# Optimization experiments

Hardware: AMD Instinct MI355X
Metric: run time of the kernel (lower is better)

## Reference

```python
import jax, jax.numpy as jnp
import numpy as np

NU = 20000; NI = 20000; E = 200000; H = 8; D = 64; F = H * D
B = 1024; P = 8; K = 8


def gat(h, W, al, ar, b, src, dst, N):
    # DGL GATConv (eval mode, dropout off): fc -> edge attention -> edge softmax -> scatter-sum -> bias -> elu
    f = (h @ W).reshape(N, H, D)                       # [N,H,D]
    el = jnp.einsum('nhd,hd->nh', f, al)               # [N,H]
    er = jnp.einsum('nhd,hd->nh', f, ar)
    e = jax.nn.leaky_relu(el[src] + er[dst], 0.2)      # [E,H]
    m = jax.ops.segment_max(e, dst, num_segments=N)    # [N,H]
    m = jnp.where(jnp.isfinite(m), m, 0.0)             # nodes w/ zero in-degree
    ex = jnp.exp(e - m[dst])                           # [E,H]
    s = jax.ops.segment_sum(ex, dst, num_segments=N)   # [N,H]
    alpha = ex / jnp.maximum(s[dst], 1e-9)             # [E,H]
    out = jax.ops.segment_sum(alpha[:, :, None] * f[src], dst, num_segments=N)  # [N,H,D]
    return jax.nn.elu(out.reshape(N, F) + b)


def semantic_attention(z, W1, b1, v):
    # z: [N, M, F]
    w = jnp.mean(jnp.tanh(z @ W1 + b1) @ v, axis=0)    # [M]
    beta = jax.nn.softmax(w)
    return jnp.einsum('m,nmf->nf', beta, z)


def han_layer(h, Wg, al, ar, bg, W1, b1, v, src, dst, N):
    zs = [gat(h, Wg[i], al[i], ar[i], bg[i], src[i], dst[i], N) for i in range(Wg.shape[0])]
    return semantic_attention(jnp.stack(zs, axis=1), W1, b1, v)


def setup_inputs() -> dict:
    key = jax.random.key(0)
    ks = jax.random.split(key, 24)
    sc = 0.05
    return {
        'user_embs': jax.random.normal(ks[0], (NU, D), jnp.float32) * sc,
        'item_embs': jax.random.normal(ks[1], (NI, D), jnp.float32) * sc,
        'Wg_u': jax.random.normal(ks[2], (2, D, F), jnp.float32) * sc,
        'al_u': jax.random.normal(ks[3], (2, H, D), jnp.float32) * sc,
        'ar_u': jax.random.normal(ks[4], (2, H, D), jnp.float32) * sc,
        'bg_u': jax.random.normal(ks[5], (2, F), jnp.float32) * sc,
        'Ws_u': jax.random.normal(ks[6], (F, 128), jnp.float32) * sc,
        'bs_u': jax.random.normal(ks[7], (128,), jnp.float32) * sc,
        'vs_u': jax.random.normal(ks[8], (128,), jnp.float32) * sc,
        'Wg_i': jax.random.normal(ks[9], (2, D, F), jnp.float32) * sc,
        'al_i': jax.random.normal(ks[10], (2, H, D), jnp.float32) * sc,
        'ar_i': jax.random.normal(ks[11], (2, H, D), jnp.float32) * sc,
        'bg_i': jax.random.normal(ks[12], (2, F), jnp.float32) * sc,
        'Ws_i': jax.random.normal(ks[13], (F, 128), jnp.float32) * sc,
        'bs_i': jax.random.normal(ks[14], (128,), jnp.float32) * sc,
        'vs_i': jax.random.normal(ks[15], (128,), jnp.float32) * sc,
        'src_u': jax.random.randint(ks[16], (2, E), 0, NU, jnp.int32),
        'dst_u': jax.random.randint(ks[17], (2, E), 0, NU, jnp.int32),
        'src_i': jax.random.randint(ks[18], (2, E), 0, NI, jnp.int32),
        'dst_i': jax.random.randint(ks[19], (2, E), 0, NI, jnp.int32),
        'uid': jax.random.randint(ks[20], (B,), 0, NU, jnp.int32),
        'pos': jax.random.randint(ks[21], (B, P), 0, NI, jnp.int32),
        'neg': jax.random.randint(ks[22], (B, P, K), 0, NI, jnp.int32),
    }


def reference(user_embs, item_embs, Wg_u, al_u, ar_u, bg_u, Ws_u, bs_u, vs_u,
              Wg_i, al_i, ar_i, bg_i, Ws_i, bs_i, vs_i,
              src_u, dst_u, src_i, dst_i, uid, pos, neg):
    hu = han_layer(user_embs, Wg_u, al_u, ar_u, bg_u, Ws_u, bs_u, vs_u, src_u, dst_u, NU)  # [NU,F]
    hi = han_layer(item_embs, Wg_i, al_i, ar_i, bg_i, Ws_i, bs_i, vs_i, src_i, dst_i, NI)  # [NI,F]
    ue = hu[uid]                                     # [B,F]
    pe = hi[pos]                                     # [B,P,F]
    ne = hi[neg]                                     # [B,P,K,F]
    ue_p = jnp.broadcast_to(ue[:, None, :], pe.shape)
    pos_logits = (ue_p * pe).sum(-1)[..., None]      # [B,P,1]
    ue_n = jnp.broadcast_to(ue_p[:, :, None, :], ne.shape)
    neg_logits = (ue_n * ne).sum(-1)                 # [B,P,K]
    return pos_logits, neg_logits, ue_n, pe, ne
```

## Files before the change

### kernel.cpp

```cpp
#include <hip/hip_runtime.h>
#include <hip/hip_bf16.h>
#include <cstddef>

#define NN 20000
#define EE 200000

typedef __attribute__((ext_vector_type(8))) short bf8_t;
typedef __attribute__((ext_vector_type(4))) float f32x4;

__device__ __forceinline__ float bf2f(unsigned int lo16) {
    return __uint_as_float(lo16 << 16);
}
__device__ __forceinline__ unsigned short f2bf(float f) {
    unsigned u = __float_as_uint(f);
    u += 0x7fffu + ((u >> 16) & 1u);
    return (unsigned short)(u >> 16);
}

__global__ void prep_kernel(
    const float* __restrict__ user_embs, const float* __restrict__ item_embs,
    const float* __restrict__ Wg_u, const float* __restrict__ Wg_i,
    const float* __restrict__ Ws_u, const float* __restrict__ Ws_i,
    unsigned short* __restrict__ hb,
    unsigned short* __restrict__ Wt,
    unsigned short* __restrict__ W1t)
{
    int i = blockIdx.x * 256 + threadIdx.x;
    if (i < 2 * NN * 64) {
        float v = (i < NN * 64) ? user_embs[i] : item_embs[i - NN * 64];
        hb[i] = f2bf(v);
    }
    if (i < 4 * 512 * 64) {
        int tg = i >> 15, rem = i & 32767;
        int col = rem >> 6, k = rem & 63;
        const float* W = (tg < 2 ? Wg_u + tg * 32768 : Wg_i + (tg - 2) * 32768);
        Wt[i] = f2bf(W[k * 512 + col]);
    }
    if (i < 2 * 128 * 512) {
        int t = i >> 16, rem = i & 65535;
        int c = rem >> 9, k = rem & 511;
        const float* Wsrc = t ? Ws_i : Ws_u;
        W1t[i] = f2bf(Wsrc[k * 128 + c]);
    }
}

__global__ __launch_bounds__(256) void fc_kernel(
    const unsigned short* __restrict__ hb,
    const unsigned short* __restrict__ Wt,
    const float* __restrict__ al_u, const float* __restrict__ ar_u,
    const float* __restrict__ al_i, const float* __restrict__ ar_i,
    unsigned short* __restrict__ fb,
    float* __restrict__ el, float* __restrict__ er)
{
    const int tg = blockIdx.y, t = tg >> 1, g = tg & 1;
    const int tid = threadIdx.x, wid = tid >> 6, lane = tid & 63;
    const int r0 = blockIdx.x * 16;
    const unsigned short* A = hb + (size_t)t * NN * 64;
    const unsigned short* B = Wt + (size_t)tg * 512 * 64;
    const float* alf = (t ? al_i : al_u) + g * 512;
    const float* arf = (t ? ar_i : ar_u) + g * 512;

    const int arow = lane & 15, ak0 = (lane >> 4) * 8;
    const bf8_t a0 = *(const bf8_t*)(A + (size_t)(r0 + arow) * 64 + ak0);
    const bf8_t a1 = *(const bf8_t*)(A + (size_t)(r0 + arow) * 64 + 32 + ak0);

    f32x4 acc[8];
#pragma unroll
    for (int i = 0; i < 8; ++i) acc[i] = f32x4{0.f, 0.f, 0.f, 0.f};

#pragma unroll
    for (int tn = 0; tn < 8; ++tn) {
        const unsigned short* bp =
            B + (size_t)(wid * 128 + tn * 16 + (lane & 15)) * 64 + ak0;
        bf8_t b0 = *(const bf8_t*)(bp);
        bf8_t b1 = *(const bf8_t*)(bp + 32);
        acc[tn] = __builtin_amdgcn_mfma_f32_16x16x32_bf16(a0, b0, acc[tn], 0, 0, 0);
        acc[tn] = __builtin_amdgcn_mfma_f32_16x16x32_bf16(a1, b1, acc[tn], 0, 0, 0);
    }

    float elp[2][4], erp[2][4];
#pragma unroll
    for (int hs = 0; hs < 2; ++hs)
#pragma unroll
        for (int r = 0; r < 4; ++r) { elp[hs][r] = 0.f; erp[hs][r] = 0.f; }

#pragma unroll
    for (int tn = 0; tn < 8; ++tn) {
        const int hs = tn >> 2;
        const int col = wid * 128 + tn * 16 + (lane & 15);
        const float av = alf[col], rv = arf[col];
#pragma unroll
        for (int r = 0; r < 4; ++r) {
            elp[hs][r] += acc[tn][r] * av;
            erp[hs][r] += acc[tn][r] * rv;
        }
    }
#pragma unroll
    for (int m = 1; m < 16; m <<= 1) {
#pragma unroll
        for (int hs = 0; hs < 2; ++hs)
#pragma unroll
            for (int r = 0; r < 4; ++r) {
                elp[hs][r] += __shfl_xor(elp[hs][r], m, 64);
                erp[hs][r] += __shfl_xor(erp[hs][r], m, 64);
            }
    }
    if ((lane & 15) == 0) {
        float* elg = el + (size_t)tg * NN * 8;
        float* erg = er + (size_t)tg * NN * 8;
#pragma unroll
        for (int r = 0; r < 4; ++r) {
            const int n = r0 + (lane >> 4) * 4 + r;
            elg[n * 8 + 2 * wid + 0] = elp[0][r];
            elg[n * 8 + 2 * wid + 1] = elp[1][r];
            erg[n * 8 + 2 * wid + 0] = erp[0][r];
            erg[n * 8 + 2 * wid + 1] = erp[1][r];
        }
    }

    __shared__ unsigned short sf[16][512];
#pragma unroll
    for (int tn = 0; tn < 8; ++tn)
#pragma unroll
        for (int r = 0; r < 4; ++r)
            sf[(lane >> 4) * 4 + r][wid * 128 + tn * 16 + (lane & 15)] =
                f2bf(acc[tn][r]);
    __syncthreads();
    unsigned short* fo = fb + (size_t)tg * NN * 512;
#pragma unroll
    for (int s = 0; s < 4; ++s) {
        int ch = tid + s * 256;
        int row = ch >> 6, off = (ch & 63) * 8;
        *(uint4*)(fo + (size_t)(r0 + row) * 512 + off) = *(uint4*)&sf[row][off];
    }
}

__global__ void zero_kernel(int* __restrict__ count, int* __restrict__ cursor,
                            float* __restrict__ wsum)
{
    int i = blockIdx.x * 256 + threadIdx.x;
    if (i < 4 * NN) { count[i] = 0; cursor[i] = 0; }
    if (i < 4) wsum[i] = 0.f;
}

__global__ void hist_kernel(const int* __restrict__ dst_u,
                            const int* __restrict__ dst_i,
                            int* __restrict__ count)
{
    int g = blockIdx.y;
    int i = blockIdx.x * 256 + threadIdx.x;
    if (i < EE) {
        const int* d = (g < 2 ? dst_u : dst_i) + (size_t)(g & 1) * EE;
        atomicAdd(&count[g * NN + d[i]], 1);
    }
}

__global__ __launch_bounds__(256) void scan1_kernel(
    const int* __restrict__ count, int* __restrict__ tmp,
    int* __restrict__ partials)
{
    const int g = blockIdx.y, tid = threadIdx.x;
    const int i = blockIdx.x * 256 + tid;
    __shared__ int sc[256];
    int v = (i < NN) ? count[g * NN + i] : 0;
    sc[tid] = v;
    __syncthreads();
#pragma unroll
    for (int off = 1; off < 256; off <<= 1) {
        int add = (tid >= off) ? sc[tid - off] : 0;
        __syncthreads();
        sc[tid] += add;
        __syncthreads();
    }
    if (i < NN) tmp[g * NN + i] = sc[tid] - v;
    if (tid == 255) partials[g * 79 + blockIdx.x] = sc[255];
}

__global__ __launch_bounds__(256) void scan2_kernel(
    const int* __restrict__ partials, int* __restrict__ bases)
{
    __shared__ int p[320], bl[320];
    const int tid = threadIdx.x;
    for (int i = tid; i < 316; i += 256) p[i] = partials[i];
    __syncthreads();
    if (tid < 4) {
        int base = 0;
        for (int b = 0; b < 79; ++b) { bl[tid * 79 + b] = base; base += p[tid * 79 + b]; }
    }
    __syncthreads();
    for (int i = tid; i < 316; i += 256) bases[i] = bl[i];
}

__global__ void scan3_kernel(const int* __restrict__ tmp,
                             const int* __restrict__ bases,
                             int* __restrict__ roff)
{
    const int g = blockIdx.y;
    const int i = blockIdx.x * 256 + threadIdx.x;
    if (i < NN) roff[g * (NN + 1) + i] = tmp[g * NN + i] + bases[g * 79 + blockIdx.x];
    if (blockIdx.x == 0 && threadIdx.x == 0) roff[g * (NN + 1) + NN] = EE;
}

__global__ void scatter_kernel(const int* __restrict__ src_u,
                               const int* __restrict__ dst_u,
                               const int* __restrict__ src_i,
                               const int* __restrict__ dst_i,
                               const int* __restrict__ roff,
                               int* __restrict__ cursor,
                               int* __restrict__ csrc)
{
    int g = blockIdx.y;
    int i = blockIdx.x * 256 + threadIdx.x;
    if (i < EE) {
        const int* s = (g < 2 ? src_u : src_i) + (size_t)(g & 1) * EE;
        const int* d = (g < 2 ? dst_u : dst_i) + (size_t)(g & 1) * EE;
        int dd = d[i];
        int pp = atomicAdd(&cursor[g * NN + dd], 1);
        csrc[(size_t)g * EE + roff[g * (NN + 1) + dd] + pp] = s[i];
    }
}

__global__ __launch_bounds__(256) void agg_kernel(
    const unsigned short* __restrict__ fb,
    const float* __restrict__ el, const float* __restrict__ er,
    const int* __restrict__ roff, const int* __restrict__ csrc,
    const float* __restrict__ bg_u, const float* __restrict__ bg_i,
    unsigned short* __restrict__ zb)
{
    const int tg = blockIdx.y, t = tg >> 1, g = tg & 1;
    const int tid = threadIdx.x, wid = tid >> 6, lane = tid & 63;
    const int n = blockIdx.x * 4 + wid;
    const unsigned short* fg = fb + (size_t)tg * NN * 512;
    const float* elg = el + (size_t)tg * NN * 8;
    const float* erg = er + (size_t)tg * NN * 8;
    const int* ro = roff + (size_t)tg * (NN + 1);
    const int* cs = csrc + (size_t)tg * EE;
    const float* bias = (t ? bg_i : bg_u) + g * 512;

    const int h = lane >> 3, c0 = lane * 8;
    const float ern = erg[n * 8 + h];
    const int beg = ro[n], end = ro[n + 1];

    float s = 0.f;
    float a0 = 0.f, a1 = 0.f, a2 = 0.f, a3 = 0.f, a4 = 0.f, a5 = 0.f, a6 = 0.f, a7 = 0.f;
    for (int e = beg; e < end; ++e) {
        int src = cs[e];
        float x = elg[src * 8 + h] + ern;
        x = (x >= 0.f) ? x : 0.2f * x;
        float ex = __expf(x);
        s += ex;
        uint4 fv = *(const uint4*)(fg + (size_t)src * 512 + c0);
        a0 += ex * bf2f(fv.x & 0xffffu);  a1 += ex * __uint_as_float(fv.x & 0xffff0000u);
        a2 += ex * bf2f(fv.y & 0xffffu);  a3 += ex * __uint_as_float(fv.y & 0xffff0000u);
        a4 += ex * bf2f(fv.z & 0xffffu);  a5 += ex * __uint_as_float(fv.z & 0xffff0000u);
        a6 += ex * bf2f(fv.w & 0xffffu);  a7 += ex * __uint_as_float(fv.w & 0xffff0000u);
    }
    const float inv = 1.f / fmaxf(s, 1e-9f);
    const float4 bA = *(const float4*)(bias + c0);
    const float4 bB = *(const float4*)(bias + c0 + 4);
    float o0 = a0 * inv + bA.x; o0 = o0 > 0.f ? o0 : expm1f(o0);
    float o1 = a1 * inv + bA.y; o1 = o1 > 0.f ? o1 : expm1f(o1);
    float o2 = a2 * inv + bA.z; o2 = o2 > 0.f ? o2 : expm1f(o2);
    float o3 = a3 * inv + bA.w; o3 = o3 > 0.f ? o3 : expm1f(o3);
    float o4 = a4 * inv + bB.x; o4 = o4 > 0.f ? o4 : expm1f(o4);
    float o5 = a5 * inv + bB.y; o5 = o5 > 0.f ? o5 : expm1f(o5);
    float o6 = a6 * inv + bB.z; o6 = o6 > 0.f ? o6 : expm1f(o6);
    float o7 = a7 * inv + bB.w; o7 = o7 > 0.f ? o7 : expm1f(o7);
    uint4 pk;
    pk.x = ((unsigned)f2bf(o1) << 16) | f2bf(o0);
    pk.y = ((unsigned)f2bf(o3) << 16) | f2bf(o2);
    pk.z = ((unsigned)f2bf(o5) << 16) | f2bf(o4);
    pk.w = ((unsigned)f2bf(o7) << 16) | f2bf(o6);
    *(uint4*)(zb + (size_t)tg * NN * 512 + (size_t)n * 512 + c0) = pk;
}

__global__ __launch_bounds__(256) void sem_kernel(
    const unsigned short* __restrict__ zb,
    const unsigned short* __restrict__ W1t,
    const float* __restrict__ bs_u, const float* __restrict__ vs_u,
    const float* __restrict__ bs_i, const float* __restrict__ vs_i,
    float* __restrict__ wsum)
{
    const int tm = blockIdx.y, t = tm >> 1;
    const int tid = threadIdx.x, wid = tid >> 6, lane = tid & 63;
    const int r0 = blockIdx.x * 32;
    const unsigned short* Az = zb + (size_t)tm * NN * 512;
    const unsigned short* Bw = W1t + (size_t)t * 128 * 512;
    const float* b1f = t ? bs_i : bs_u;
    const float* vf  = t ? vs_i : vs_u;

    const int arow = lane & 15, ak0 = (lane >> 4) * 8;
    const int col0 = wid * 32 + (lane & 15);
    const unsigned short* a0p = Az + (size_t)(r0 + arow) * 512 + ak0;
    const unsigned short* a1p = a0p + 16 * 512;
    const unsigned short* b0p = Bw + (size_t)col0 * 512 + ak0;
    const unsigned short* b1p = b0p + 16 * 512;

    f32x4 acc00 = f32x4{0.f,0.f,0.f,0.f}, acc01 = acc00, acc10 = acc00, acc11 = acc00;
#pragma unroll 4
    for (int k = 0; k < 512; k += 32) {
        bf8_t a0 = *(const bf8_t*)(a0p + k);
        bf8_t a1 = *(const bf8_t*)(a1p + k);
        bf8_t b0 = *(const bf8_t*)(b0p + k);
        bf8_t b1 = *(const bf8_t*)(b1p + k);
        acc00 = __builtin_amdgcn_mfma_f32_16x16x32_bf16(a0, b0, acc00, 0, 0, 0);
        acc01 = __builtin_amdgcn_mfma_f32_16x16x32_bf16(a0, b1, acc01, 0, 0, 0);
        acc10 = __builtin_amdgcn_mfma_f32_16x16x32_bf16(a1, b0, acc10, 0, 0, 0);
        acc11 = __builtin_amdgcn_mfma_f32_16x16x32_bf16(a1, b1, acc11, 0, 0, 0);
    }

    const float b1c0 = b1f[col0], b1c1 = b1f[col0 + 16];
    const float vc0 = vf[col0],  vc1 = vf[col0 + 16];
    float q = 0.f;
#pragma unroll
    for (int r = 0; r < 4; ++r) {
        q += tanhf(acc00[r] + b1c0) * vc0;
        q += tanhf(acc01[r] + b1c1) * vc1;
        q += tanhf(acc10[r] + b1c0) * vc0;
        q += tanhf(acc11[r] + b1c1) * vc1;
    }
#pragma unroll
    for (int m = 1; m < 64; m <<= 1) q += __shfl_xor(q, m, 64);
    __shared__ float red[4];
    if (lane == 0) red[wid] = q;
    __syncthreads();
    if (tid == 0) atomicAdd(&wsum[tm], red[0] + red[1] + red[2] + red[3]);
}

__global__ void combine_kernel(const unsigned short* __restrict__ zb,
                               const float* __restrict__ wsum,
                               float* __restrict__ hu, float* __restrict__ hi)
{
    const int t = blockIdx.y;
    const float w0 = wsum[2 * t] * (1.f / (float)NN);
    const float w1 = wsum[2 * t + 1] * (1.f / (float)NN);
    const float m = fmaxf(w0, w1);
    const float e0 = __expf(w0 - m), e1 = __expf(w1 - m);
    const float is = 1.f / (e0 + e1);
    const float be0 = e0 * is, be1 = e1 * is;

    const size_t idx = (size_t)blockIdx.x * 256 + threadIdx.x;
    const unsigned short* z0 = zb + (size_t)(2 * t) * NN * 512 + idx * 8;
    const unsigned short* z1 = zb + (size_t)(2 * t + 1) * NN * 512 + idx * 8;
    float* ho = (t ? hi : hu) + idx * 8;
    uint4 u0 = *(const uint4*)z0;
    uint4 u1 = *(const uint4*)z1;
    float4 oA, oB;
    oA.x = be0 * bf2f(u0.x & 0xffffu) + be1 * bf2f(u1.x & 0xffffu);
    oA.y = be0 * __uint_as_float(u0.x & 0xffff0000u) + be1 * __uint_as_float(u1.x & 0xffff0000u);
    oA.z = be0 * bf2f(u0.y & 0xffffu) + be1 * bf2f(u1.y & 0xffffu);
    oA.w = be0 * __uint_as_float(u0.y & 0xffff0000u) + be1 * __uint_as_float(u1.y & 0xffff0000u);
    oB.x = be0 * bf2f(u0.z & 0xffffu) + be1 * bf2f(u1.z & 0xffffu);
    oB.y = be0 * __uint_as_float(u0.z & 0xffff0000u) + be1 * __uint_as_float(u1.z & 0xffff0000u);
    oB.z = be0 * bf2f(u0.w & 0xffffu) + be1 * bf2f(u1.w & 0xffffu);
    oB.w = be0 * __uint_as_float(u0.w & 0xffff0000u) + be1 * __uint_as_float(u1.w & 0xffff0000u);
    *(float4*)(ho) = oA;
    *(float4*)(ho + 4) = oB;
}

__global__ __launch_bounds__(128) void score_kernel(
    const float* __restrict__ hu, const float* __restrict__ hi,
    const int* __restrict__ uid, const int* __restrict__ pos,
    const int* __restrict__ neg, float* __restrict__ out)
{
    const int bp  = blockIdx.x;
    const int b   = bp >> 3;
    const int tid = threadIdx.x;
    __shared__ float red[2];

    float* pos_logits = out;
    float* neg_logits = out + 8192;
    float* ue_n       = out + 73728;
    float* pe         = out + 33628160;
    float* ne         = out + 37822464;

    const float4 u4 = ((const float4*)(hu + (size_t)uid[b] * 512))[tid];

    {
        const float4 p4 = ((const float4*)(hi + (size_t)pos[bp] * 512))[tid];
        ((float4*)(pe + (size_t)bp * 512))[tid] = p4;
        float d = u4.x * p4.x + u4.y * p4.y + u4.z * p4.z + u4.w * p4.w;
#pragma unroll
        for (int off = 32; off; off >>= 1) d += __shfl_down(d, off, 64);
        if ((tid & 63) == 0) red[tid >> 6] = d;
        __syncthreads();
        if (tid == 0) pos_logits[bp] = red[0] + red[1];
    }
    for (int k = 0; k < 8; ++k) {
        __syncthreads();
        const size_t row = (size_t)bp * 8 + k;
        const float4 n4 = ((const float4*)(hi + (size_t)neg[row] * 512))[tid];
        ((float4*)(ne   + row * 512))[tid] = n4;
        ((float4*)(ue_n + row * 512))[tid] = u4;
        float d = u4.x * n4.x + u4.y * n4.y + u4.z * n4.z + u4.w * n4.w;
#pragma unroll
        for (int off = 32; off; off >>= 1) d += __shfl_down(d, off, 64);
        if ((tid & 63) == 0) red[tid >> 6] = d;
        __syncthreads();
        if (tid == 0) neg_logits[row] = red[0] + red[1];
    }
}

extern "C" void kernel_launch(void* const* d_in, const int* in_sizes, int n_in,
                              void* d_out, int out_size, void* d_ws, size_t ws_size,
                              hipStream_t stream)
{
    const float* user_embs = (const float*)d_in[0];
    const float* item_embs = (const float*)d_in[1];
    const float* Wg_u = (const float*)d_in[2];
    const float* al_u = (const float*)d_in[3];
    const float* ar_u = (const float*)d_in[4];
    const float* bg_u = (const float*)d_in[5];
    const float* Ws_u = (const float*)d_in[6];
    const float* bs_u = (const float*)d_in[7];
    const float* vs_u = (const float*)d_in[8];
    const float* Wg_i = (const float*)d_in[9];
    const float* al_i = (const float*)d_in[10];
    const float* ar_i = (const float*)d_in[11];
    const float* bg_i = (const float*)d_in[12];
    const float* Ws_i = (const float*)d_in[13];
    const float* bs_i = (const float*)d_in[14];
    const float* vs_i = (const float*)d_in[15];
    const int* src_u = (const int*)d_in[16];
    const int* dst_u = (const int*)d_in[17];
    const int* src_i = (const int*)d_in[18];
    const int* dst_i = (const int*)d_in[19];
    const int* uid = (const int*)d_in[20];
    const int* pos = (const int*)d_in[21];
    const int* neg = (const int*)d_in[22];

    char* p = (char*)d_ws;
    auto carve = [&](size_t bytes) {
        char* r = p; p += (bytes + 255) & ~(size_t)255; return r;
    };
    unsigned short* fb  = (unsigned short*)carve((size_t)4 * NN * 512 * 2);
    unsigned short* zb  = (unsigned short*)carve((size_t)4 * NN * 512 * 2);
    unsigned short* hb  = (unsigned short*)carve((size_t)2 * NN * 64 * 2);
    unsigned short* Wt  = (unsigned short*)carve((size_t)4 * 512 * 64 * 2);
    unsigned short* W1t = (unsigned short*)carve((size_t)2 * 128 * 512 * 2);
    float* el   = (float*)carve((size_t)4 * NN * 8 * 4);
    float* er   = (float*)carve((size_t)4 * NN * 8 * 4);
    float* wsum = (float*)carve(64);
    int* count    = (int*)carve((size_t)4 * NN * 4);
    int* cursor   = (int*)carve((size_t)4 * NN * 4);
    int* tmp      = (int*)carve((size_t)4 * NN * 4);
    int* roff     = (int*)carve((size_t)4 * (NN + 1) * 4);
    int* partials = (int*)carve(320 * 4);
    int* bases    = (int*)carve(320 * 4);
    int* csrc     = (int*)carve((size_t)4 * EE * 4);
    float* hu = (float*)fb;
    float* hi = hu + (size_t)NN * 512;

    prep_kernel<<<(2 * NN * 64 + 255) / 256, 256, 0, stream>>>(
        user_embs, item_embs, Wg_u, Wg_i, Ws_u, Ws_i, hb, Wt, W1t);
    zero_kernel<<<(4 * NN + 255) / 256, 256, 0, stream>>>(count, cursor, wsum);
    hist_kernel<<<dim3((EE + 255) / 256, 4), 256, 0, stream>>>(dst_u, dst_i, count);
    scan1_kernel<<<dim3(79, 4), 256, 0, stream>>>(count, tmp, partials);
    scan2_kernel<<<1, 256, 0, stream>>>(partials, bases);
    scan3_kernel<<<dim3(79, 4), 256, 0, stream>>>(tmp, bases, roff);
    scatter_kernel<<<dim3((EE + 255) / 256, 4), 256, 0, stream>>>(
        src_u, dst_u, src_i, dst_i, roff, cursor, csrc);
    fc_kernel<<<dim3(NN / 16, 4), 256, 0, stream>>>(
        hb, Wt, al_u, ar_u, al_i, ar_i, fb, el, er);
    agg_kernel<<<dim3(NN / 4, 4), 256, 0, stream>>>(
        fb, el, er, roff, csrc, bg_u, bg_i, zb);
    sem_kernel<<<dim3(NN / 32, 4), 256, 0, stream>>>(
        zb, W1t, bs_u, vs_u, bs_i, vs_i, wsum);
    combine_kernel<<<dim3(NN * 512 / 8 / 256, 2), 256, 0, stream>>>(zb, wsum, hu, hi);
    score_kernel<<<1024 * 8, 128, 0, stream>>>(hu, hi, uid, pos, neg, (float*)d_out);
}
```

Before: 717.2 us.

## Fuse semantic combine into score kernel and fold zeroing into prep

Removes the combine kernel that built full fp32 hu/hi tables for every node. The score kernel now reads only the gathered rows of the two bf16 metapath embeddings and blends them with the semantic softmax weights on the fly, using one wave per block and no shared-memory reduction. The zero kernel is also merged into prep to save a launch. This avoids writing and re-reading about 80 MB of fp32 node embeddings, at the cost of reading two bf16 rows per gather and recomputing the softmax weights in every block.

```diff
diff --git a/kernel.cpp b/kernel.cpp
--- a/kernel.cpp
+++ b/kernel.cpp
@@ -10,6 +10,9 @@
 
 __device__ __forceinline__ float bf2f(unsigned int lo16) {
     return __uint_as_float(lo16 << 16);
+}
+__device__ __forceinline__ float hi16f(unsigned int u) {
+    return __uint_as_float(u & 0xffff0000u);
 }
 __device__ __forceinline__ unsigned short f2bf(float f) {
     unsigned u = __float_as_uint(f);
@@ -23,7 +26,9 @@
     const float* __restrict__ Ws_u, const float* __restrict__ Ws_i,
     unsigned short* __restrict__ hb,
     unsigned short* __restrict__ Wt,
-    unsigned short* __restrict__ W1t)
+    unsigned short* __restrict__ W1t,
+    int* __restrict__ count, int* __restrict__ cursor,
+    float* __restrict__ wsum)
 {
     int i = blockIdx.x * 256 + threadIdx.x;
     if (i < 2 * NN * 64) {
@@ -42,6 +47,8 @@
         const float* Wsrc = t ? Ws_i : Ws_u;
         W1t[i] = f2bf(Wsrc[k * 128 + c]);
     }
+    if (i < 4 * NN) { count[i] = 0; cursor[i] = 0; }
+    if (i < 4) wsum[i] = 0.f;
 }
 
 __global__ __launch_bounds__(256) void fc_kernel(
@@ -133,14 +140,6 @@
         int row = ch >> 6, off = (ch & 63) * 8;
         *(uint4*)(fo + (size_t)(r0 + row) * 512 + off) = *(uint4*)&sf[row][off];
     }
-}
-
-__global__ void zero_kernel(int* __restrict__ count, int* __restrict__ cursor,
-                            float* __restrict__ wsum)
-{
-    int i = blockIdx.x * 256 + threadIdx.x;
-    if (i < 4 * NN) { count[i] = 0; cursor[i] = 0; }
-    if (i < 4) wsum[i] = 0.f;
 }
 
 __global__ void hist_kernel(const int* __restrict__ dst_u,
@@ -250,10 +249,10 @@
         float ex = __expf(x);
         s += ex;
         uint4 fv = *(const uint4*)(fg + (size_t)src * 512 + c0);
-        a0 += ex * bf2f(fv.x & 0xffffu);  a1 += ex * __uint_as_float(fv.x & 0xffff0000u);
-        a2 += ex * bf2f(fv.y & 0xffffu);  a3 += ex * __uint_as_float(fv.y & 0xffff0000u);
-        a4 += ex * bf2f(fv.z & 0xffffu);  a5 += ex * __uint_as_float(fv.z & 0xffff0000u);
-        a6 += ex * bf2f(fv.w & 0xffffu);  a7 += ex * __uint_as_float(fv.w & 0xffff0000u);
+        a0 += ex * bf2f(fv.x & 0xffffu);  a1 += ex * hi16f(fv.x);
+        a2 += ex * bf2f(fv.y & 0xffffu);  a3 += ex * hi16f(fv.y);
+        a4 += ex * bf2f(fv.z & 0xffffu);  a5 += ex * hi16f(fv.z);
+        a6 += ex * bf2f(fv.w & 0xffffu);  a7 += ex * hi16f(fv.w);
     }
     const float inv = 1.f / fmaxf(s, 1e-9f);
     const float4 bA = *(const float4*)(bias + c0);
@@ -327,46 +326,44 @@
     if (tid == 0) atomicAdd(&wsum[tm], red[0] + red[1] + red[2] + red[3]);
 }
 
-__global__ void combine_kernel(const unsigned short* __restrict__ zb,
-                               const float* __restrict__ wsum,
-                               float* __restrict__ hu, float* __restrict__ hi)
-{
-    const int t = blockIdx.y;
-    const float w0 = wsum[2 * t] * (1.f / (float)NN);
-    const float w1 = wsum[2 * t + 1] * (1.f / (float)NN);
-    const float m = fmaxf(w0, w1);
-    const float e0 = __expf(w0 - m), e1 = __expf(w1 - m);
-    const float is = 1.f / (e0 + e1);
-    const float be0 = e0 * is, be1 = e1 * is;
-
-    const size_t idx = (size_t)blockIdx.x * 256 + threadIdx.x;
-    const unsigned short* z0 = zb + (size_t)(2 * t) * NN * 512 + idx * 8;
-    const unsigned short* z1 = zb + (size_t)(2 * t + 1) * NN * 512 + idx * 8;
-    float* ho = (t ? hi : hu) + idx * 8;
-    uint4 u0 = *(const uint4*)z0;
-    uint4 u1 = *(const uint4*)z1;
-    float4 oA, oB;
-    oA.x = be0 * bf2f(u0.x & 0xffffu) + be1 * bf2f(u1.x & 0xffffu);
-    oA.y = be0 * __uint_as_float(u0.x & 0xffff0000u) + be1 * __uint_as_float(u1.x & 0xffff0000u);
-    oA.z = be0 * bf2f(u0.y & 0xffffu) + be1 * bf2f(u1.y & 0xffffu);
-    oA.w = be0 * __uint_as_float(u0.y & 0xffff0000u) + be1 * __uint_as_float(u1.y & 0xffff0000u);
-    oB.x = be0 * bf2f(u0.z & 0xffffu) + be1 * bf2f(u1.z & 0xffffu);
-    oB.y = be0 * __uint_as_float(u0.z & 0xffff0000u) + be1 * __uint_as_float(u1.z & 0xffff0000u);
-    oB.z = be0 * bf2f(u0.w & 0xffffu) + be1 * bf2f(u1.w & 0xffffu);
-    oB.w = be0 * __uint_as_float(u0.w & 0xffff0000u) + be1 * __uint_as_float(u1.w & 0xffff0000u);
-    *(float4*)(ho) = oA;
-    *(float4*)(ho + 4) = oB;
-}
-
-__global__ __launch_bounds__(128) void score_kernel(
-    const float* __restrict__ hu, const float* __restrict__ hi,
+__device__ __forceinline__ void comb8(uint4 q0, uint4 q1, float b0, float b1,
+                                      float* __restrict__ o)
+{
+    o[0] = b0 * bf2f(q0.x & 0xffffu) + b1 * bf2f(q1.x & 0xffffu);
+    o[1] = b0 * hi16f(q0.x)          + b1 * hi16f(q1.x);
+    o[2] = b0 * bf2f(q0.y & 0xffffu) + b1 * bf2f(q1.y & 0xffffu);
+    o[3] = b0 * hi16f(q0.y)          + b1 * hi16f(q1.y);
+    o[4] = b0 * bf2f(q0.z & 0xffffu) + b1 * bf2f(q1.z & 0xffffu);
+    o[5] = b0 * hi16f(q0.z)          + b1 * hi16f(q1.z);
+    o[6] = b0 * bf2f(q0.w & 0xffffu) + b1 * bf2f(q1.w & 0xffffu);
+    o[7] = b0 * hi16f(q0.w)          + b1 * hi16f(q1.w);
+}
+
+__global__ __launch_bounds__(64) void score_kernel(
+    const unsigned short* __restrict__ zb,
+    const float* __restrict__ wsum,
     const int* __restrict__ uid, const int* __restrict__ pos,
     const int* __restrict__ neg, float* __restrict__ out)
 {
-    const int bp  = blockIdx.x;
-    const int b   = bp >> 3;
-    const int tid = threadIdx.x;
-    __shared__ float red[2];
+    const int bp = blockIdx.x, b = bp >> 3;
+    const int lane = threadIdx.x;
+    const int c0 = lane * 8;
+
+    const float wu0 = wsum[0] * (1.f / (float)NN), wu1 = wsum[1] * (1.f / (float)NN);
+    const float mu = fmaxf(wu0, wu1);
+    const float eu0 = __expf(wu0 - mu), eu1 = __expf(wu1 - mu);
+    const float su = 1.f / (eu0 + eu1);
+    const float bu0 = eu0 * su, bu1 = eu1 * su;
+    const float wi0 = wsum[2] * (1.f / (float)NN), wi1 = wsum[3] * (1.f / (float)NN);
+    const float mi = fmaxf(wi0, wi1);
+    const float ei0 = __expf(wi0 - mi), ei1 = __expf(wi1 - mi);
+    const float si = 1.f / (ei0 + ei1);
+    const float bi0 = ei0 * si, bi1 = ei1 * si;
+
+    const unsigned short* zu0 = zb;
+    const unsigned short* zu1 = zb + (size_t)NN * 512;
+    const unsigned short* zi0 = zb + (size_t)2 * NN * 512;
+    const unsigned short* zi1 = zb + (size_t)3 * NN * 512;
 
     float* pos_logits = out;
     float* neg_logits = out + 8192;
@@ -374,30 +371,42 @@
     float* pe         = out + 33628160;
     float* ne         = out + 37822464;
 
-    const float4 u4 = ((const float4*)(hu + (size_t)uid[b] * 512))[tid];
-
+    float u[8];
     {
-        const float4 p4 = ((const float4*)(hi + (size_t)pos[bp] * 512))[tid];
-        ((float4*)(pe + (size_t)bp * 512))[tid] = p4;
-        float d = u4.x * p4.x + u4.y * p4.y + u4.z * p4.z + u4.w * p4.w;
-#pragma unroll
-        for (int off = 32; off; off >>= 1) d += __shfl_down(d, off, 64);
-        if ((tid & 63) == 0) red[tid >> 6] = d;
-        __syncthreads();
-        if (tid == 0) pos_logits[bp] = red[0] + red[1];
-    }
+        const size_t off = (size_t)uid[b] * 512 + c0;
+        comb8(*(const uint4*)(zu0 + off), *(const uint4*)(zu1 + off), bu0, bu1, u);
+    }
+
+    {
+        const size_t off = (size_t)pos[bp] * 512 + c0;
+        float pv[8];
+        comb8(*(const uint4*)(zi0 + off), *(const uint4*)(zi1 + off), bi0, bi1, pv);
+        float* pr = pe + (size_t)bp * 512 + c0;
+        *(float4*)(pr)     = make_float4(pv[0], pv[1], pv[2], pv[3]);
+        *(float4*)(pr + 4) = make_float4(pv[4], pv[5], pv[6], pv[7]);
+        float d = u[0]*pv[0] + u[1]*pv[1] + u[2]*pv[2] + u[3]*pv[3]
+                + u[4]*pv[4] + u[5]*pv[5] + u[6]*pv[6] + u[7]*pv[7];
+#pragma unroll
+        for (int off2 = 32; off2; off2 >>= 1) d += __shfl_down(d, off2, 64);
+        if (lane == 0) pos_logits[bp] = d;
+    }
+
     for (int k = 0; k < 8; ++k) {
-        __syncthreads();
         const size_t row = (size_t)bp * 8 + k;
-        const float4 n4 = ((const float4*)(hi + (size_t)neg[row] * 512))[tid];
-        ((float4*)(ne   + row * 512))[tid] = n4;
-        ((float4*)(ue_n + row * 512))[tid] = u4;
-        float d = u4.x * n4.x + u4.y * n4.y + u4.z * n4.z + u4.w * n4.w;
-#pragma unroll
-        for (int off = 32; off; off >>= 1) d += __shfl_down(d, off, 64);
-        if ((tid & 63) == 0) red[tid >> 6] = d;
-        __syncthreads();
-        if (tid == 0) neg_logits[row] = red[0] + red[1];
+        const size_t off = (size_t)neg[row] * 512 + c0;
+        float nv[8];
+        comb8(*(const uint4*)(zi0 + off), *(const uint4*)(zi1 + off), bi0, bi1, nv);
+        float* nr = ne + row * 512 + c0;
+        *(float4*)(nr)     = make_float4(nv[0], nv[1], nv[2], nv[3]);
+        *(float4*)(nr + 4) = make_float4(nv[4], nv[5], nv[6], nv[7]);
+        float* ur = ue_n + row * 512 + c0;
+        *(float4*)(ur)     = make_float4(u[0], u[1], u[2], u[3]);
+        *(float4*)(ur + 4) = make_float4(u[4], u[5], u[6], u[7]);
+        float d = u[0]*nv[0] + u[1]*nv[1] + u[2]*nv[2] + u[3]*nv[3]
+                + u[4]*nv[4] + u[5]*nv[5] + u[6]*nv[6] + u[7]*nv[7];
+#pragma unroll
+        for (int off2 = 32; off2; off2 >>= 1) d += __shfl_down(d, off2, 64);
+        if (lane == 0) neg_logits[row] = d;
     }
 }
 
@@ -448,12 +457,10 @@
     int* partials = (int*)carve(320 * 4);
     int* bases    = (int*)carve(320 * 4);
     int* csrc     = (int*)carve((size_t)4 * EE * 4);
-    float* hu = (float*)fb;
-    float* hi = hu + (size_t)NN * 512;
 
     prep_kernel<<<(2 * NN * 64 + 255) / 256, 256, 0, stream>>>(
-        user_embs, item_embs, Wg_u, Wg_i, Ws_u, Ws_i, hb, Wt, W1t);
-    zero_kernel<<<(4 * NN + 255) / 256, 256, 0, stream>>>(count, cursor, wsum);
+        user_embs, item_embs, Wg_u, Wg_i, Ws_u, Ws_i, hb, Wt, W1t,
+        count, cursor, wsum);
     hist_kernel<<<dim3((EE + 255) / 256, 4), 256, 0, stream>>>(dst_u, dst_i, count);
     scan1_kernel<<<dim3(79, 4), 256, 0, stream>>>(count, tmp, partials);
     scan2_kernel<<<1, 256, 0, stream>>>(partials, bases);
@@ -466,6 +473,5 @@
         fb, el, er, roff, csrc, bg_u, bg_i, zb);
     sem_kernel<<<dim3(NN / 32, 4), 256, 0, stream>>>(
         zb, W1t, bs_u, vs_u, bs_i, vs_i, wsum);
-    combine_kernel<<<dim3(NN * 512 / 8 / 256, 2), 256, 0, stream>>>(zb, wsum, hu, hi);
-    score_kernel<<<1024 * 8, 128, 0, stream>>>(hu, hi, uid, pos, neg, (float*)d_out);
-}
+    score_kernel<<<1024 * 8, 64, 0, stream>>>(zb, wsum, uid, pos, neg, (float*)d_out);
+}
```

Result: faster. 691.8 us (-3.5%).
